# Optimization experiments

Measured on AMD Instinct MI355X. Metric: run time of the kernel, lower is better.

The kernel has to match this reference:

```python
import jax, jax.numpy as jnp
import numpy as np

B, D, N, K = 256, 1024, 200000, 64  # batch, model_dim, n_slots, outer_dim
EPS = 1e-8


def setup_inputs() -> dict:
    key = jax.random.key(0)
    k1, k2, k3, k4, k5 = jax.random.split(key, 5)
    return {
        "cue": jax.random.normal(k1, (B, D), dtype=jnp.float32),
        "slot_matrix": jax.random.normal(k2, (N, K), dtype=jnp.float32),
        "priority": jax.random.uniform(k3, (N,), dtype=jnp.float32),
        "w_cue": jax.random.normal(k4, (K, D), dtype=jnp.float32) * (1.0 / np.sqrt(D)),
        "w_dec": jax.random.normal(k5, (D, K), dtype=jnp.float32) * (1.0 / np.sqrt(K)),
    }


def reference(cue, slot_matrix, priority, w_cue, w_dec):
    # cue_proj: (B, D) @ (D, K) -> (B, K)
    cue_outer = jnp.einsum('bd,kd->bk', cue, w_cue)
    # dot-product similarity against every slot: (B, N)
    sim = jnp.einsum('bk,nk->bn', cue_outer, slot_matrix)
    weights = jax.nn.softmax(sim, axis=-1)
    # priority-modulated renormalization
    weights = weights * priority[None, :]
    weights = weights / jnp.clip(weights.sum(axis=-1, keepdims=True), EPS)
    # weighted readout over slots: (B, K)
    retrieved = jnp.einsum('bn,nk->bk', weights, slot_matrix)
    # decoder: (B, K) @ (K, D) -> (B, D)
    return jnp.einsum('bk,dk->bd', retrieved, w_dec)
```

## Files before the change

kernel.cpp:

```cpp
#include <hip/hip_runtime.h>
#include <hip/hip_fp16.h>

#define B_ 256
#define D_ 1024
#define N_ 200000
#define K_ 64
#define SHIFT_ 24.0f
#define NCHUNK 3125

typedef short short8 __attribute__((ext_vector_type(8)));
typedef _Float16 f16x8 __attribute__((ext_vector_type(8)));
typedef float f32x4 __attribute__((ext_vector_type(4)));

__device__ __forceinline__ unsigned f2bf(float x) {
  unsigned u = __float_as_uint(x);
  return (u + 0x7fffu + ((u >> 16) & 1u)) >> 16;
}
__device__ __forceinline__ unsigned pack2(float a, float b) {
  return f2bf(a) | (f2bf(b) << 16);
}
__device__ __forceinline__ float bf2f(unsigned short u) {
  return __uint_as_float(((unsigned)u) << 16);
}
__device__ __forceinline__ unsigned f2h(float x) {
  return (unsigned)__half_as_ushort(__float2half(x));
}
__device__ __forceinline__ f32x4 mfma16b(int4 a, int4 b, f32x4 c) {
  return __builtin_amdgcn_mfma_f32_16x16x32_bf16(
      __builtin_bit_cast(short8, a), __builtin_bit_cast(short8, b), c, 0, 0, 0);
}
__device__ __forceinline__ f32x4 mfma16h(int4 a, int4 b, f32x4 c) {
  return __builtin_amdgcn_mfma_f32_16x16x32_f16(
      __builtin_bit_cast(f16x8, a), __builtin_bit_cast(f16x8, b), c, 0, 0, 0);
}
__device__ __forceinline__ int p8hash(int k) { return ((k >> 3) ^ k) & 7; }

__global__ __launch_bounds__(256) void k1_cueproj(
    const float* __restrict__ cue, const float* __restrict__ wcue,
    float* __restrict__ couter) {
  const int b    = blockIdx.x;
  const int tid  = threadIdx.x;
  const int w    = tid >> 6;
  const int lane = tid & 63;

  __shared__ float part[4][64][65];
  __shared__ float red[4][64];

  const float4 creg =
      *(const float4*)(cue + (size_t)b * D_ + w * 256 + lane * 4);
  const float* wbase = wcue + w * 256 + lane * 4;

#pragma unroll 8
  for (int k = 0; k < 64; ++k) {
    const float4 wv = *(const float4*)(wbase + (size_t)k * D_);
    part[w][k][lane] =
        creg.x * wv.x + creg.y * wv.y + creg.z * wv.z + creg.w * wv.w;
  }
  __syncthreads();

  const int k  = tid & 63;
  const int wq = tid >> 6;
  float a = 0.f;
#pragma unroll 8
  for (int j = 0; j < 64; ++j) a += part[wq][k][j];
  red[wq][k] = a;
  __syncthreads();
  if (tid < 64) {
    couter[b * K_ + tid] =
        red[0][tid] + red[1][tid] + red[2][tid] + red[3][tid];
  }
}

__global__ __launch_bounds__(256, 2) void k2_attend(
    const float* __restrict__ slot, const float* __restrict__ prio,
    const float* __restrict__ couter, unsigned short* __restrict__ Spart,
    float* __restrict__ Zpart, int G) {
  __shared__ __align__(16) unsigned short sh_h[64 * 72];
  __shared__ __align__(16) unsigned short sh_T[64 * 64];
  __shared__ __align__(16) unsigned short sh_E[4 * 64 * 72];
  __shared__ float sh_p[64];

  const int tid = threadIdx.x;
  const int g   = blockIdx.x;
  const int l   = tid & 63;
  const int w   = tid >> 6;
  const int c16 = l & 15;
  const int q   = l >> 4;

  int4 qf[4][2];
#pragma unroll
  for (int bt = 0; bt < 4; ++bt) {
#pragma unroll
    for (int s = 0; s < 2; ++s) {
      const float* qp =
          couter + (size_t)(w * 64 + bt * 16 + c16) * K_ + s * 32 + q * 8;
      float4 va = *(const float4*)qp;
      float4 vb = *(const float4*)(qp + 4);
      qf[bt][s] = make_int4(
          (int)(f2h(va.x) | (f2h(va.y) << 16)),
          (int)(f2h(va.z) | (f2h(va.w) << 16)),
          (int)(f2h(vb.x) | (f2h(vb.y) << 16)),
          (int)(f2h(vb.z) | (f2h(vb.w) << 16)));
    }
  }

  f32x4 S[4][4];
#pragma unroll
  for (int a = 0; a < 4; ++a)
#pragma unroll
    for (int b = 0; b < 4; ++b) S[a][b] = (f32x4){0.f, 0.f, 0.f, 0.f};
  float zacc[4] = {0.f, 0.f, 0.f, 0.f};

  float4 pf[4];
  float ppf = 0.f;
  {
    const float4* src = (const float4*)(slot + (size_t)g * 64 * K_);
#pragma unroll
    for (int i = 0; i < 4; ++i) pf[i] = src[tid + 256 * i];
    if (tid < 64) ppf = prio[g * 64 + tid];
  }

  for (int chunk = g; chunk < NCHUNK; chunk += G) {
    __syncthreads();
#pragma unroll
    for (int i = 0; i < 4; ++i) {
      const int f   = tid + 256 * i;
      const int row = f >> 4;
      const int c4  = (f & 15) * 4;
      float xs[4] = {pf[i].x, pf[i].y, pf[i].z, pf[i].w};
      unsigned hh[4];
#pragma unroll
      for (int j = 0; j < 4; ++j) {
        hh[j] = f2h(xs[j]);
        const int k = c4 + j;
        sh_T[k * 64 + (row ^ (p8hash(k) << 3))] =
            (unsigned short)f2bf(xs[j]);
      }
      *(uint2*)&sh_h[row * 72 + c4] =
          make_uint2(hh[0] | (hh[1] << 16), hh[2] | (hh[3] << 16));
    }
    if (tid < 64) sh_p[tid] = ppf;
    __syncthreads();

    const int nxt = chunk + G;
    if (nxt < NCHUNK) {
      const float4* src = (const float4*)(slot + (size_t)nxt * 64 * K_);
#pragma unroll
      for (int i = 0; i < 4; ++i) pf[i] = src[tid + 256 * i];
      if (tid < 64) ppf = prio[nxt * 64 + tid];
    }

#pragma unroll
    for (int t = 0; t < 4; ++t) {
      f32x4 cc[4];
#pragma unroll
      for (int bt = 0; bt < 4; ++bt) cc[bt] = (f32x4){0.f, 0.f, 0.f, 0.f};
#pragma unroll
      for (int s = 0; s < 2; ++s) {
        const int off = (t * 16 + c16) * 72 + s * 32 + q * 8;
        int4 ah = *(const int4*)&sh_h[off];
#pragma unroll
        for (int bt = 0; bt < 4; ++bt) cc[bt] = mfma16h(ah, qf[bt][s], cc[bt]);
      }
      const float4 p = *(const float4*)&sh_p[t * 16 + q * 4];
#pragma unroll
      for (int bt = 0; bt < 4; ++bt) {
        float e0 = __expf(cc[bt][0] - SHIFT_) * p.x;
        float e1 = __expf(cc[bt][1] - SHIFT_) * p.y;
        float e2 = __expf(cc[bt][2] - SHIFT_) * p.z;
        float e3 = __expf(cc[bt][3] - SHIFT_) * p.w;
        zacc[bt] += (e0 + e1) + (e2 + e3);
        *(uint2*)&sh_E[w * 4608 + (bt * 16 + c16) * 72 + t * 16 + q * 4] =
            make_uint2(pack2(e0, e1), pack2(e2, e3));
      }
    }

#pragma unroll
    for (int s = 0; s < 2; ++s) {
      int4 bT[4];
#pragma unroll
      for (int ct = 0; ct < 4; ++ct) {
        const int k = ct * 16 + c16;
        bT[ct] = *(const int4*)&sh_T[k * 64 +
                                     ((s * 32 + q * 8) ^ (p8hash(k) << 3))];
      }
#pragma unroll
      for (int bt = 0; bt < 4; ++bt) {
        int4 aE = *(const int4*)&sh_E[w * 4608 + (bt * 16 + c16) * 72 +
                                      s * 32 + q * 8];
#pragma unroll
        for (int ct = 0; ct < 4; ++ct)
          S[bt][ct] = mfma16b(aE, bT[ct], S[bt][ct]);
      }
    }
  }

#pragma unroll
  for (int bt = 0; bt < 4; ++bt) {
#pragma unroll
    for (int ct = 0; ct < 4; ++ct) {
#pragma unroll
      for (int r = 0; r < 4; ++r) {
        sh_E[(w * 64 + bt * 16 + q * 4 + r) * 72 + ct * 16 + c16] =
            (unsigned short)f2bf(S[bt][ct][r]);
      }
    }
  }
  __syncthreads();
#pragma unroll
  for (int i = 0; i < 8; ++i) {
    const int idx   = tid + 256 * i;
    const int batch = idx >> 3;
    const int seg   = idx & 7;
    uint4 v = *(const uint4*)&sh_E[batch * 72 + seg * 8];
    *(uint4*)&Spart[((size_t)batch * G + g) * K_ + seg * 8] = v;
  }
#pragma unroll
  for (int bt = 0; bt < 4; ++bt) {
    float z = zacc[bt];
    z += __shfl_xor(z, 16);
    z += __shfl_xor(z, 32);
    if (l < 16) Zpart[(size_t)(w * 64 + bt * 16 + c16) * G + g] = z;
  }
}

__global__ __launch_bounds__(256) void k3_decode(
    const unsigned short* __restrict__ Spart, const float* __restrict__ Zpart,
    const float* __restrict__ wdec, float* __restrict__ out, int G) {
  const int b   = blockIdx.x;
  const int tid = threadIdx.x;
  const int k = tid & 63, grp = tid >> 6;

  __shared__ float red[4][K_];
  __shared__ float zred[256];
  __shared__ float rk[K_];
  __shared__ float wlds[256 * 65];

  const unsigned short* sp = Spart + (size_t)b * G * K_;
  float s = 0.f;
  for (int g = grp; g < G; g += 4) s += bf2f(sp[(size_t)g * K_ + k]);
  red[grp][k] = s;

  float zp = 0.f;
  const float* zpp = Zpart + (size_t)b * G;
  for (int g = tid; g < G; g += 256) zp += zpp[g];
  zred[tid] = zp;
  __syncthreads();

  if (tid < K_) {
    float ssum = red[0][k] + red[1][k] + red[2][k] + red[3][k];
    if (tid == 0) {
      float zz = 0.f;
      for (int i = 0; i < 256; ++i) zz += zred[i];
      zred[0] = fmaxf(zz, 1e-30f);
    }
    red[0][k] = ssum;
  }
  __syncthreads();
  if (tid < K_) rk[tid] = red[0][k] / zred[0];

  for (int d0 = 0; d0 < D_; d0 += 256) {
    __syncthreads();
#pragma unroll
    for (int i = 0; i < 16; ++i) {
      const int f   = tid + 256 * i;
      const int row = f >> 4;
      const int c4  = (f & 15) * 4;
      const float4 v = *(const float4*)(wdec + (size_t)(d0 + row) * K_ + c4);
      wlds[row * 65 + c4 + 0] = v.x;
      wlds[row * 65 + c4 + 1] = v.y;
      wlds[row * 65 + c4 + 2] = v.z;
      wlds[row * 65 + c4 + 3] = v.w;
    }
    __syncthreads();
    float acc = 0.f;
#pragma unroll
    for (int kk = 0; kk < 64; ++kk) acc += rk[kk] * wlds[tid * 65 + kk];
    out[(size_t)b * D_ + d0 + tid] = acc;
  }
}

extern "C" void kernel_launch(void* const* d_in, const int* in_sizes, int n_in,
                              void* d_out, int out_size, void* d_ws,
                              size_t ws_size, hipStream_t stream) {
  const float* cue  = (const float*)d_in[0];
  const float* slot = (const float*)d_in[1];
  const float* prio = (const float*)d_in[2];
  const float* wcue = (const float*)d_in[3];
  const float* wdec = (const float*)d_in[4];
  float* out = (float*)d_out;

  const size_t per_g = (size_t)B_ * K_ * 2 + (size_t)B_ * 4;
  long long avail = (long long)ws_size - 65536;
  int G = (int)(avail > 0 ? avail / (long long)per_g : 1);
  if (G > 512) G = 512;
  if (G < 1) G = 1;

  float* couter         = (float*)d_ws;
  unsigned short* Spart = (unsigned short*)(couter + 16384);
  float* Zpart          = (float*)(Spart + (size_t)B_ * G * K_);

  k1_cueproj<<<dim3(B_), dim3(256), 0, stream>>>(cue, wcue, couter);
  k2_attend<<<dim3(G), dim3(256), 0, stream>>>(slot, prio, couter, Spart,
                                               Zpart, G);
  k3_decode<<<dim3(B_), dim3(256), 0, stream>>>(Spart, Zpart, wdec, out, G);
}
```

Measured before the change: 158.3 us.

## Split decode into sliced partial reduction and D-parallel decode kernels

The final stage is split into two kernels. The first reduces the per-group bf16 partials across 8 slices per batch, reading them with 16-byte vector loads. The second decodes across 4 column blocks per batch instead of looping over D inside one block. This raises the number of workgroups in the tail stage and widens memory accesses, at the cost of an extra kernel launch, a small workspace buffer, and rounding G down to a multiple of 8.

```diff
diff --git a/kernel.cpp b/kernel.cpp
--- a/kernel.cpp
+++ b/kernel.cpp
@@ -7,6 +7,7 @@
 #define K_ 64
 #define SHIFT_ 24.0f
 #define NCHUNK 3125
+#define SL_ 8
 
 typedef short short8 __attribute__((ext_vector_type(8)));
 typedef _Float16 f16x8 __attribute__((ext_vector_type(8)));
@@ -224,22 +225,55 @@
   }
 }
 
-__global__ __launch_bounds__(256) void k3_decode(
-    const unsigned short* __restrict__ Spart, const float* __restrict__ Zpart,
+__global__ __launch_bounds__(256) void k3a_reduce(
+    const unsigned short* __restrict__ Spart, float* __restrict__ rkpart,
+    int G) {
+  const int b   = blockIdx.x;
+  const int s   = blockIdx.y;
+  const int tid = threadIdx.x;
+  const int gq  = tid >> 3;
+  const int k8  = tid & 7;
+
+  __shared__ float part[32][65];
+
+  const int gcnt = G / SL_;
+  const int gbeg = s * gcnt;
+
+  float acc[8] = {0.f, 0.f, 0.f, 0.f, 0.f, 0.f, 0.f, 0.f};
+  const unsigned short* sp = Spart + (size_t)b * G * K_ + k8 * 8;
+  for (int gg = gq; gg < gcnt; gg += 32) {
+    uint4 v = *(const uint4*)(sp + (size_t)(gbeg + gg) * K_);
+    acc[0] += __uint_as_float(v.x << 16);
+    acc[1] += __uint_as_float(v.x & 0xffff0000u);
+    acc[2] += __uint_as_float(v.y << 16);
+    acc[3] += __uint_as_float(v.y & 0xffff0000u);
+    acc[4] += __uint_as_float(v.z << 16);
+    acc[5] += __uint_as_float(v.z & 0xffff0000u);
+    acc[6] += __uint_as_float(v.w << 16);
+    acc[7] += __uint_as_float(v.w & 0xffff0000u);
+  }
+#pragma unroll
+  for (int j = 0; j < 8; ++j) part[gq][k8 * 8 + j] = acc[j];
+  __syncthreads();
+
+  if (tid < 64) {
+    float sum = 0.f;
+#pragma unroll
+    for (int r = 0; r < 32; ++r) sum += part[r][tid];
+    rkpart[((size_t)b * SL_ + s) * K_ + tid] = sum;
+  }
+}
+
+__global__ __launch_bounds__(256) void k3b_decode(
+    const float* __restrict__ rkpart, const float* __restrict__ Zpart,
     const float* __restrict__ wdec, float* __restrict__ out, int G) {
   const int b   = blockIdx.x;
+  const int j   = blockIdx.y;
   const int tid = threadIdx.x;
-  const int k = tid & 63, grp = tid >> 6;
-
-  __shared__ float red[4][K_];
+
   __shared__ float zred[256];
   __shared__ float rk[K_];
   __shared__ float wlds[256 * 65];
-
-  const unsigned short* sp = Spart + (size_t)b * G * K_;
-  float s = 0.f;
-  for (int g = grp; g < G; g += 4) s += bf2f(sp[(size_t)g * K_ + k]);
-  red[grp][k] = s;
 
   float zp = 0.f;
   const float* zpp = Zpart + (size_t)b * G;
@@ -248,36 +282,38 @@
   __syncthreads();
 
   if (tid < K_) {
-    float ssum = red[0][k] + red[1][k] + red[2][k] + red[3][k];
+    float ssum = 0.f;
+#pragma unroll
+    for (int s = 0; s < SL_; ++s)
+      ssum += rkpart[((size_t)b * SL_ + s) * K_ + tid];
     if (tid == 0) {
       float zz = 0.f;
       for (int i = 0; i < 256; ++i) zz += zred[i];
       zred[0] = fmaxf(zz, 1e-30f);
     }
-    red[0][k] = ssum;
-  }
-  __syncthreads();
-  if (tid < K_) rk[tid] = red[0][k] / zred[0];
-
-  for (int d0 = 0; d0 < D_; d0 += 256) {
-    __syncthreads();
-#pragma unroll
-    for (int i = 0; i < 16; ++i) {
-      const int f   = tid + 256 * i;
-      const int row = f >> 4;
-      const int c4  = (f & 15) * 4;
-      const float4 v = *(const float4*)(wdec + (size_t)(d0 + row) * K_ + c4);
-      wlds[row * 65 + c4 + 0] = v.x;
-      wlds[row * 65 + c4 + 1] = v.y;
-      wlds[row * 65 + c4 + 2] = v.z;
-      wlds[row * 65 + c4 + 3] = v.w;
-    }
-    __syncthreads();
-    float acc = 0.f;
-#pragma unroll
-    for (int kk = 0; kk < 64; ++kk) acc += rk[kk] * wlds[tid * 65 + kk];
-    out[(size_t)b * D_ + d0 + tid] = acc;
-  }
+    rk[tid] = ssum;
+  }
+  __syncthreads();
+  const float invZ = 1.0f / zred[0];
+
+#pragma unroll
+  for (int i = 0; i < 16; ++i) {
+    const int f   = tid + 256 * i;
+    const int row = f >> 4;
+    const int c4  = (f & 15) * 4;
+    const float4 v =
+        *(const float4*)(wdec + (size_t)(j * 256 + row) * K_ + c4);
+    wlds[row * 65 + c4 + 0] = v.x;
+    wlds[row * 65 + c4 + 1] = v.y;
+    wlds[row * 65 + c4 + 2] = v.z;
+    wlds[row * 65 + c4 + 3] = v.w;
+  }
+  __syncthreads();
+
+  float acc = 0.f;
+#pragma unroll
+  for (int kk = 0; kk < 64; ++kk) acc += rk[kk] * wlds[tid * 65 + kk];
+  out[(size_t)b * D_ + j * 256 + tid] = acc * invZ;
 }
 
 extern "C" void kernel_launch(void* const* d_in, const int* in_sizes, int n_in,
@@ -291,17 +327,21 @@
   float* out = (float*)d_out;
 
   const size_t per_g = (size_t)B_ * K_ * 2 + (size_t)B_ * 4;
-  long long avail = (long long)ws_size - 65536;
-  int G = (int)(avail > 0 ? avail / (long long)per_g : 1);
+  long long avail = (long long)ws_size - 65536 - 524288;
+  int G = (int)(avail > 0 ? avail / (long long)per_g : SL_);
   if (G > 512) G = 512;
-  if (G < 1) G = 1;
+  G &= ~(SL_ - 1);
+  if (G < SL_) G = SL_;
 
   float* couter         = (float*)d_ws;
   unsigned short* Spart = (unsigned short*)(couter + 16384);
   float* Zpart          = (float*)(Spart + (size_t)B_ * G * K_);
+  float* rkpart         = Zpart + (size_t)B_ * G;
 
   k1_cueproj<<<dim3(B_), dim3(256), 0, stream>>>(cue, wcue, couter);
   k2_attend<<<dim3(G), dim3(256), 0, stream>>>(slot, prio, couter, Spart,
                                                Zpart, G);
-  k3_decode<<<dim3(B_), dim3(256), 0, stream>>>(Spart, Zpart, wdec, out, G);
-}
+  k3a_reduce<<<dim3(B_, SL_), dim3(256), 0, stream>>>(Spart, rkpart, G);
+  k3b_decode<<<dim3(B_, 4), dim3(256), 0, stream>>>(rkpart, Zpart, wdec, out,
+                                                    G);
+}
```

Result: faster. 134.6 us (-15.0%).
